# Optimization experiments

Measured on AMD Instinct MI355X. Metric: run time of the kernel, lower is better.

Reference implementation:

```python
import jax, jax.numpy as jnp
import numpy as np

HEADS = 8
HEAD_DIM = 64
IN_DIM = HEADS * HEAD_DIM  # 512
SCALE = HEAD_DIM ** (-0.5)


def _split_heads(t):
    # [b, n, h*d] -> [b, h, n, d]
    b, n, _ = t.shape
    return t.reshape(b, n, HEADS, HEAD_DIM).transpose(0, 2, 1, 3)


def _merge_heads(t):
    # [b, h, n, d] -> [b, n, h*d]
    b, h, n, d = t.shape
    return t.transpose(0, 2, 1, 3).reshape(b, n, h * d)


def setup_inputs() -> dict:
    key = jax.random.key(0)
    ks = jax.random.split(key, 6)
    b, n = 8, 1024
    nv = jax.random.normal(ks[0], (b, n, IN_DIM), dtype=jnp.float32)
    rv = jax.random.normal(ks[1], (b, n, IN_DIM), dtype=jnp.float32)
    s = IN_DIM ** (-0.5)
    W_noise = jax.random.normal(ks[2], (IN_DIM, 2 * IN_DIM), dtype=jnp.float32) * s
    b_noise = jnp.zeros((2 * IN_DIM,), dtype=jnp.float32)
    W_rgb = jax.random.normal(ks[3], (IN_DIM, 2 * IN_DIM), dtype=jnp.float32) * s
    b_rgb = jnp.zeros((2 * IN_DIM,), dtype=jnp.float32)
    return {"nv": nv, "rv": rv, "W_noise": W_noise, "b_noise": b_noise,
            "W_rgb": W_rgb, "b_rgb": b_rgb}


def reference(nv, rv, W_noise, b_noise, W_rgb, b_rgb):
    # qk projections, chunk(2, dim=-1)
    nqk = nv @ W_noise + b_noise                      # [b, n, 2*in_dim]
    noise_q, noise_k = jnp.split(nqk, 2, axis=-1)
    rqk = rv @ W_rgb + b_rgb
    rgb_q, rgb_k = jnp.split(rqk, 2, axis=-1)

    noise_q, noise_k = _split_heads(noise_q), _split_heads(noise_k)  # [b,h,n,d]
    rgb_q, rgb_k = _split_heads(rgb_q), _split_heads(rgb_k)

    attn1 = jnp.einsum('bhnd,bhmd->bhnm', noise_q, rgb_k) * SCALE
    attn2 = jnp.einsum('bhnd,bhmd->bhnm', rgb_q, noise_k) * SCALE

    # NOTE: original uses nn.Softmax(dim=1) => softmax over the HEADS axis.
    attn1 = jax.nn.softmax(attn1, axis=1)
    attn2 = jax.nn.softmax(attn2, axis=1)

    rv_h = _split_heads(rv)  # values are the raw inputs, not projections
    nv_h = _split_heads(nv)

    noise = jnp.einsum('bhnm,bhmd->bhnd', attn1, rv_h)
    rgb = jnp.einsum('bhnm,bhmd->bhnd', attn2, nv_h)

    return (_merge_heads(noise), _merge_heads(rgb))
```

## Files before the change

### kernel.cpp

```cpp
#include <hip/hip_runtime.h>
#include <hip/hip_bf16.h>

typedef __attribute__((ext_vector_type(8))) short short8;
typedef __attribute__((ext_vector_type(4))) short short4v;
typedef __attribute__((ext_vector_type(4))) float float4v;

#define MFMA16(a, b, c) __builtin_amdgcn_mfma_f32_16x16x32_bf16(a, b, c, 0, 0, 0)

__device__ __forceinline__ short f2bf(float f) {
    __hip_bfloat16 hb = __float2bfloat16(f);
    return *reinterpret_cast<short*>(&hb);
}

__global__ __launch_bounds__(256) void proj_kernel(
    const float* __restrict__ nv, const float* __restrict__ rv,
    const float* __restrict__ Wn, const float* __restrict__ bn,
    const float* __restrict__ Wr, const float* __restrict__ br,
    __hip_bfloat16* __restrict__ Qn, __hip_bfloat16* __restrict__ Kn,
    __hip_bfloat16* __restrict__ Qr, __hip_bfloat16* __restrict__ Kr)
{
    const int m0 = blockIdx.x * 64;
    const int c0 = blockIdx.y * 128;
    const int g  = blockIdx.z;
    const float* A    = g ? rv : nv;
    const float* W    = g ? Wr : Wn;
    const float* bias = g ? br : bn;
    __hip_bfloat16* Qd = g ? Qr : Qn;
    __hip_bfloat16* Kd = g ? Kr : Kn;

    __shared__ short Bt[128][40];

    const int t    = threadIdx.x;
    const int lane = t & 63;
    const int w    = t >> 6;
    const int l15  = lane & 15;
    const int lg   = lane >> 4;
    const int kgrp = lg * 8;

    float4v acc[8] = {};
    const int mrow = m0 + w * 16 + l15;

    for (int kk = 0; kk < 512; kk += 32) {
        {
            const int ci = t & 127;
            const int kh = (t >> 7) * 16;
            #pragma unroll
            for (int ki = 0; ki < 16; ++ki) {
                float v = W[(kk + kh + ki) * 1024 + c0 + ci];
                Bt[ci][kh + ki] = f2bf(v);
            }
        }
        __syncthreads();
        short8 afrag;
        {
            const float* ap = A + (size_t)mrow * 512 + kk + kgrp;
            float4 a0 = *reinterpret_cast<const float4*>(ap);
            float4 a1 = *reinterpret_cast<const float4*>(ap + 4);
            short* af = (short*)&afrag;
            af[0] = f2bf(a0.x); af[1] = f2bf(a0.y); af[2] = f2bf(a0.z); af[3] = f2bf(a0.w);
            af[4] = f2bf(a1.x); af[5] = f2bf(a1.y); af[6] = f2bf(a1.z); af[7] = f2bf(a1.w);
        }
        #pragma unroll
        for (int cs = 0; cs < 8; ++cs) {
            short8 bfrag = *reinterpret_cast<const short8*>(&Bt[cs * 16 + l15][kgrp]);
            acc[cs] = MFMA16(afrag, bfrag, acc[cs]);
        }
        __syncthreads();
    }

    #pragma unroll
    for (int cs = 0; cs < 8; ++cs) {
        const int c  = c0 + cs * 16 + l15;
        const bool isK = (c >= 512);
        const int hh = (c >> 6) & 7;
        const int d  = c & 63;
        __hip_bfloat16* dst = isK ? Kd : Qd;
        const float bv = bias[c];
        #pragma unroll
        for (int r = 0; r < 4; ++r) {
            const int m = m0 + w * 16 + lg * 4 + r;
            const int b = m >> 10, n = m & 1023;
            dst[(((size_t)(b * 8 + hh) * 1024 + n) * 64) + d] =
                __float2bfloat16(acc[cs][r] + bv);
        }
    }
}

__global__ __launch_bounds__(256) void transpose_kernel(
    const float* __restrict__ nv, const float* __restrict__ rv,
    __hip_bfloat16* __restrict__ Vtn, __hip_bfloat16* __restrict__ Vtr)
{
    const int ntile = blockIdx.x & 15;
    const int src   = blockIdx.x >> 4;
    const int h     = blockIdx.y;
    const int b     = blockIdx.z;
    const float* V  = src ? rv : nv;
    __hip_bfloat16* Vt = src ? Vtr : Vtn;

    __shared__ short lds[64][72];
    const int t  = threadIdx.x;
    const int n0 = ntile * 64;
    {
        const int i  = t >> 2;
        const int j0 = (t & 3) * 16;
        const float* p = V + ((size_t)(b * 1024) + n0 + i) * 512 + h * 64 + j0;
        #pragma unroll
        for (int jj = 0; jj < 16; ++jj)
            lds[j0 + jj][i] = f2bf(p[jj]);
    }
    __syncthreads();
    {
        const int j  = t >> 2;
        const int i0 = (t & 3) * 16;
        __hip_bfloat16* q = Vt + (((size_t)(b * 8 + h) * 64) + j) * 1024 + n0 + i0;
        short8 v0 = *reinterpret_cast<const short8*>(&lds[j][i0]);
        short8 v1 = *reinterpret_cast<const short8*>(&lds[j][i0 + 8]);
        *reinterpret_cast<short8*>(q)     = v0;
        *reinterpret_cast<short8*>(q + 8) = v1;
    }
}

__global__ __launch_bounds__(512, 2) void attn_kernel(
    const __hip_bfloat16* __restrict__ Qn, const __hip_bfloat16* __restrict__ Kn,
    const __hip_bfloat16* __restrict__ Qr, const __hip_bfloat16* __restrict__ Kr,
    const __hip_bfloat16* __restrict__ Vtn, const __hip_bfloat16* __restrict__ Vtr,
    float* __restrict__ out)
{
    const int combo = blockIdx.x;
    const int bb    = combo & 7;
    const int dir   = combo >> 3;
    const int nt    = blockIdx.y;
    const __hip_bfloat16* Q  = dir ? Qr  : Qn;
    const __hip_bfloat16* K  = dir ? Kn  : Kr;
    const __hip_bfloat16* Vt = dir ? Vtn : Vtr;
    float* O = out + (size_t)dir * (8u * 1024u * 512u);

    const int t    = threadIdx.x;
    const int lane = t & 63;
    const int w    = t >> 6;
    const int iw   = w & 1;
    const int hg   = w >> 1;
    const int h0   = hg * 2;
    const int l15  = lane & 15;
    const int lg   = lane >> 4;

    __shared__ short K_s[2][8 * 32 * 64];
    __shared__ short P_s[8][32][40];
    __shared__ float X_s[2][4][2][512];

    const int n0 = nt * 64;
    const float C = 0.125f * 1.44269504f;

    const __hip_bfloat16* Vb[2] = {
        Vt + (size_t)((bb * 8 + h0)     * 64) * 1024,
        Vt + (size_t)((bb * 8 + h0 + 1) * 64) * 1024 };

    auto stage = [&](int bufn, int mt) {
        #pragma unroll
        for (int i = 0; i < 4; ++i) {
            const int u    = (w * 4 + i) * 64 + lane;
            const int h    = u >> 8;
            const int mr   = (u >> 3) & 31;
            const int slot = (u & 7) ^ (mr & 7);
            const __hip_bfloat16* g =
                K + ((size_t)((bb * 8 + h) * 1024) + mt + mr) * 64 + slot * 8;
            __builtin_amdgcn_global_load_lds(
                (const __attribute__((address_space(1))) unsigned int*)g,
                (__attribute__((address_space(3))) unsigned int*)&K_s[bufn][u * 8],
                16, 0, 0);
        }
    };

    short8 qf[2][2][2];
    #pragma unroll
    for (int ns = 0; ns < 2; ++ns)
        #pragma unroll
        for (int hh = 0; hh < 2; ++hh)
            #pragma unroll
            for (int kc = 0; kc < 2; ++kc)
                qf[ns][hh][kc] = *reinterpret_cast<const short8*>(
                    Q + ((size_t)((bb * 8 + h0 + hh) * 1024) + n0 + ns * 32 + iw * 16 + l15) * 64
                      + kc * 32 + lg * 8);

    float4v oacc[2][2][4] = {};

    stage(0, 0);
    __syncthreads();

    for (int it = 0; it < 32; ++it) {
        const int m0  = it << 5;
        const int buf = it & 1;
        short8 vf[2][4];
        #pragma unroll
        for (int hh = 0; hh < 2; ++hh)
            #pragma unroll
            for (int dd = 0; dd < 4; ++dd)
                vf[hh][dd] = *reinterpret_cast<const short8*>(
                    Vb[hh] + (size_t)(dd * 16 + l15) * 1024 + m0 + lg * 8);
        short8 kf[2][2][2];
        const short* ks = K_s[buf];
        #pragma unroll
        for (int hh = 0; hh < 2; ++hh)
            #pragma unroll
            for (int j = 0; j < 2; ++j) {
                const int mr = j * 16 + l15;
                #pragma unroll
                for (int kc = 0; kc < 2; ++kc)
                    kf[hh][j][kc] = *reinterpret_cast<const short8*>(
                        ks + (h0 + hh) * 2048 + mr * 64
                           + (((kc * 4 + lg) ^ (mr & 7)) * 8));
            }

        #pragma unroll
        for (int ns = 0; ns < 2; ++ns) {
            float4v sacc[2][2] = {};
            #pragma unroll
            for (int hh = 0; hh < 2; ++hh)
                #pragma unroll
                for (int j = 0; j < 2; ++j)
                    #pragma unroll
                    for (int kc = 0; kc < 2; ++kc)
                        sacc[hh][j] = MFMA16(kf[hh][j][kc], qf[ns][hh][kc], sacc[hh][j]);
            float e[2][8];
            float ps[8] = {0.f, 0.f, 0.f, 0.f, 0.f, 0.f, 0.f, 0.f};
            #pragma unroll
            for (int hh = 0; hh < 2; ++hh)
                #pragma unroll
                for (int j = 0; j < 2; ++j)
                    #pragma unroll
                    for (int r = 0; r < 4; ++r) {
                        float ev = exp2f(sacc[hh][j][r] * C);
                        e[hh][j * 4 + r] = ev;
                        ps[j * 4 + r] += ev;
                    }
            #pragma unroll
            for (int p = 0; p < 8; ++p)
                X_s[ns][hg][iw][p * 64 + lane] = ps[p];
            __syncthreads();
            if (ns == 0)
                stage(buf ^ 1, (it < 31) ? m0 + 32 : 0);
            float inv[8];
            #pragma unroll
            for (int p = 0; p < 8; ++p) {
                float tot = ps[p];
                #pragma unroll
                for (int g = 1; g < 4; ++g)
                    tot += X_s[ns][(hg + g) & 3][iw][p * 64 + lane];
                inv[p] = __builtin_amdgcn_rcpf(tot);
            }
            #pragma unroll
            for (int hh = 0; hh < 2; ++hh)
                #pragma unroll
                for (int j = 0; j < 2; ++j) {
                    short4v pk;
                    #pragma unroll
                    for (int r = 0; r < 4; ++r)
                        pk[r] = f2bf(e[hh][j * 4 + r] * inv[j * 4 + r]);
                    *reinterpret_cast<short4v*>(
                        &P_s[h0 + hh][iw * 16 + l15][j * 16 + lg * 4]) = pk;
                }
            #pragma unroll
            for (int hh = 0; hh < 2; ++hh) {
                short8 pf = *reinterpret_cast<const short8*>(
                    &P_s[h0 + hh][iw * 16 + l15][lg * 8]);
                #pragma unroll
                for (int dd = 0; dd < 4; ++dd)
                    oacc[ns][hh][dd] = MFMA16(pf, vf[hh][dd], oacc[ns][hh][dd]);
            }
        }
        __syncthreads();
    }

    #pragma unroll
    for (int ns = 0; ns < 2; ++ns)
        #pragma unroll
        for (int hh = 0; hh < 2; ++hh)
            #pragma unroll
            for (int dd = 0; dd < 4; ++dd)
                #pragma unroll
                for (int r = 0; r < 4; ++r) {
                    const int n = n0 + ns * 32 + iw * 16 + lg * 4 + r;
                    const int d = dd * 16 + l15;
                    O[((size_t)(bb * 1024) + n) * 512 + (h0 + hh) * 64 + d] =
                        oacc[ns][hh][dd][r];
                }
}

extern "C" void kernel_launch(void* const* d_in, const int* in_sizes, int n_in,
                              void* d_out, int out_size, void* d_ws, size_t ws_size,
                              hipStream_t stream) {
    const float* nv = (const float*)d_in[0];
    const float* rv = (const float*)d_in[1];
    const float* Wn = (const float*)d_in[2];
    const float* bn = (const float*)d_in[3];
    const float* Wr = (const float*)d_in[4];
    const float* br = (const float*)d_in[5];
    float* out = (float*)d_out;

    __hip_bfloat16* w = (__hip_bfloat16*)d_ws;
    const size_t E = 8ull * 8 * 1024 * 64;
    __hip_bfloat16* Qn  = w;
    __hip_bfloat16* Kn  = w + E;
    __hip_bfloat16* Qr  = w + 2 * E;
    __hip_bfloat16* Kr  = w + 3 * E;
    __hip_bfloat16* Vtn = w + 4 * E;
    __hip_bfloat16* Vtr = w + 5 * E;

    proj_kernel<<<dim3(128, 8, 2), 256, 0, stream>>>(nv, rv, Wn, bn, Wr, br, Qn, Kn, Qr, Kr);
    transpose_kernel<<<dim3(32, 8, 8), 256, 0, stream>>>(nv, rv, Vtn, Vtr);
    attn_kernel<<<dim3(16, 16), 512, 0, stream>>>(Qn, Kn, Qr, Kr, Vtn, Vtr, out);
}
```

Measured before the change: 173.9 us.

## Pre-convert weights and inputs to bf16, double-buffer projection GEMM, trim attention syncs

Measured after the change: 179.3 us. +3.1%, slower.

```diff
diff --git a/kernel.cpp b/kernel.cpp
--- a/kernel.cpp
+++ b/kernel.cpp
@@ -12,83 +12,42 @@
     return *reinterpret_cast<short*>(&hb);
 }
 
-__global__ __launch_bounds__(256) void proj_kernel(
+__global__ __launch_bounds__(256) void wt_kernel(
+    const float* __restrict__ Wn, const float* __restrict__ Wr,
+    __hip_bfloat16* __restrict__ Wtn, __hip_bfloat16* __restrict__ Wtr)
+{
+    const int c0 = blockIdx.x * 64;
+    const int k0 = blockIdx.y * 64;
+    const int g  = blockIdx.z;
+    const float* W = g ? Wr : Wn;
+    __hip_bfloat16* Wt = g ? Wtr : Wtn;
+
+    __shared__ short lds[64][72];
+    const int t = threadIdx.x;
+    {
+        const int i  = t >> 2;
+        const int j0 = (t & 3) * 16;
+        const float* p = W + (size_t)(k0 + i) * 1024 + c0 + j0;
+        #pragma unroll
+        for (int jj = 0; jj < 16; ++jj)
+            lds[j0 + jj][i] = f2bf(p[jj]);
+    }
+    __syncthreads();
+    {
+        const int j  = t >> 2;
+        const int i0 = (t & 3) * 16;
+        __hip_bfloat16* q = Wt + (size_t)(c0 + j) * 512 + k0 + i0;
+        short8 v0 = *reinterpret_cast<const short8*>(&lds[j][i0]);
+        short8 v1 = *reinterpret_cast<const short8*>(&lds[j][i0 + 8]);
+        *reinterpret_cast<short8*>(q)     = v0;
+        *reinterpret_cast<short8*>(q + 8) = v1;
+    }
+}
+
+__global__ __launch_bounds__(256) void prep_kernel(
     const float* __restrict__ nv, const float* __restrict__ rv,
-    const float* __restrict__ Wn, const float* __restrict__ bn,
-    const float* __restrict__ Wr, const float* __restrict__ br,
-    __hip_bfloat16* __restrict__ Qn, __hip_bfloat16* __restrict__ Kn,
-    __hip_bfloat16* __restrict__ Qr, __hip_bfloat16* __restrict__ Kr)
-{
-    const int m0 = blockIdx.x * 64;
-    const int c0 = blockIdx.y * 128;
-    const int g  = blockIdx.z;
-    const float* A    = g ? rv : nv;
-    const float* W    = g ? Wr : Wn;
-    const float* bias = g ? br : bn;
-    __hip_bfloat16* Qd = g ? Qr : Qn;
-    __hip_bfloat16* Kd = g ? Kr : Kn;
-
-    __shared__ short Bt[128][40];
-
-    const int t    = threadIdx.x;
-    const int lane = t & 63;
-    const int w    = t >> 6;
-    const int l15  = lane & 15;
-    const int lg   = lane >> 4;
-    const int kgrp = lg * 8;
-
-    float4v acc[8] = {};
-    const int mrow = m0 + w * 16 + l15;
-
-    for (int kk = 0; kk < 512; kk += 32) {
-        {
-            const int ci = t & 127;
-            const int kh = (t >> 7) * 16;
-            #pragma unroll
-            for (int ki = 0; ki < 16; ++ki) {
-                float v = W[(kk + kh + ki) * 1024 + c0 + ci];
-                Bt[ci][kh + ki] = f2bf(v);
-            }
-        }
-        __syncthreads();
-        short8 afrag;
-        {
-            const float* ap = A + (size_t)mrow * 512 + kk + kgrp;
-            float4 a0 = *reinterpret_cast<const float4*>(ap);
-            float4 a1 = *reinterpret_cast<const float4*>(ap + 4);
-            short* af = (short*)&afrag;
-            af[0] = f2bf(a0.x); af[1] = f2bf(a0.y); af[2] = f2bf(a0.z); af[3] = f2bf(a0.w);
-            af[4] = f2bf(a1.x); af[5] = f2bf(a1.y); af[6] = f2bf(a1.z); af[7] = f2bf(a1.w);
-        }
-        #pragma unroll
-        for (int cs = 0; cs < 8; ++cs) {
-            short8 bfrag = *reinterpret_cast<const short8*>(&Bt[cs * 16 + l15][kgrp]);
-            acc[cs] = MFMA16(afrag, bfrag, acc[cs]);
-        }
-        __syncthreads();
-    }
-
-    #pragma unroll
-    for (int cs = 0; cs < 8; ++cs) {
-        const int c  = c0 + cs * 16 + l15;
-        const bool isK = (c >= 512);
-        const int hh = (c >> 6) & 7;
-        const int d  = c & 63;
-        __hip_bfloat16* dst = isK ? Kd : Qd;
-        const float bv = bias[c];
-        #pragma unroll
-        for (int r = 0; r < 4; ++r) {
-            const int m = m0 + w * 16 + lg * 4 + r;
-            const int b = m >> 10, n = m & 1023;
-            dst[(((size_t)(b * 8 + hh) * 1024 + n) * 64) + d] =
-                __float2bfloat16(acc[cs][r] + bv);
-        }
-    }
-}
-
-__global__ __launch_bounds__(256) void transpose_kernel(
-    const float* __restrict__ nv, const float* __restrict__ rv,
-    __hip_bfloat16* __restrict__ Vtn, __hip_bfloat16* __restrict__ Vtr)
+    __hip_bfloat16* __restrict__ Vtn, __hip_bfloat16* __restrict__ Vtr,
+    __hip_bfloat16* __restrict__ An,  __hip_bfloat16* __restrict__ Ar)
 {
     const int ntile = blockIdx.x & 15;
     const int src   = blockIdx.x >> 4;
@@ -96,6 +55,7 @@
     const int b     = blockIdx.z;
     const float* V  = src ? rv : nv;
     __hip_bfloat16* Vt = src ? Vtr : Vtn;
+    __hip_bfloat16* Ab = src ? Ar  : An;
 
     __shared__ short lds[64][72];
     const int t  = threadIdx.x;
@@ -104,9 +64,20 @@
         const int i  = t >> 2;
         const int j0 = (t & 3) * 16;
         const float* p = V + ((size_t)(b * 1024) + n0 + i) * 512 + h * 64 + j0;
-        #pragma unroll
-        for (int jj = 0; jj < 16; ++jj)
-            lds[j0 + jj][i] = f2bf(p[jj]);
+        short8 a0, a1;
+        #pragma unroll
+        for (int jj = 0; jj < 8; ++jj) {
+            short x = f2bf(p[jj]);
+            a0[jj] = x; lds[j0 + jj][i] = x;
+        }
+        #pragma unroll
+        for (int jj = 0; jj < 8; ++jj) {
+            short x = f2bf(p[8 + jj]);
+            a1[jj] = x; lds[j0 + 8 + jj][i] = x;
+        }
+        __hip_bfloat16* adst = Ab + ((size_t)(b * 1024) + n0 + i) * 512 + h * 64 + j0;
+        *reinterpret_cast<short8*>(adst)     = a0;
+        *reinterpret_cast<short8*>(adst + 8) = a1;
     }
     __syncthreads();
     {
@@ -117,6 +88,82 @@
         short8 v1 = *reinterpret_cast<const short8*>(&lds[j][i0 + 8]);
         *reinterpret_cast<short8*>(q)     = v0;
         *reinterpret_cast<short8*>(q + 8) = v1;
+    }
+}
+
+__global__ __launch_bounds__(256, 4) void proj_kernel(
+    const __hip_bfloat16* __restrict__ An, const __hip_bfloat16* __restrict__ Ar,
+    const __hip_bfloat16* __restrict__ Wtn, const __hip_bfloat16* __restrict__ Wtr,
+    const float* __restrict__ bn, const float* __restrict__ br,
+    __hip_bfloat16* __restrict__ Qn, __hip_bfloat16* __restrict__ Kn,
+    __hip_bfloat16* __restrict__ Qr, __hip_bfloat16* __restrict__ Kr)
+{
+    const int m0 = blockIdx.x * 64;
+    const int c0 = blockIdx.y * 128;
+    const int g  = blockIdx.z;
+    const __hip_bfloat16* A  = g ? Ar  : An;
+    const __hip_bfloat16* Wt = g ? Wtr : Wtn;
+    const float* bias = g ? br : bn;
+    __hip_bfloat16* Qd = g ? Qr : Qn;
+    __hip_bfloat16* Kd = g ? Kr : Kn;
+
+    __shared__ short Bt[2][4][128][8];
+
+    const int t    = threadIdx.x;
+    const int lane = t & 63;
+    const int w    = t >> 6;
+    const int l15  = lane & 15;
+    const int lg   = lane >> 4;
+
+    auto stage = [&](int buf, int kk) {
+        #pragma unroll
+        for (int rep = 0; rep < 2; ++rep) {
+            const int u = rep * 256 + t;
+            const int s = u >> 7;
+            const int c = u & 127;
+            const __hip_bfloat16* src = Wt + (size_t)(c0 + c) * 512 + kk + s * 8;
+            __builtin_amdgcn_global_load_lds(
+                (const __attribute__((address_space(1))) unsigned int*)src,
+                (__attribute__((address_space(3))) unsigned int*)&Bt[buf][s][c][0],
+                16, 0, 0);
+        }
+    };
+
+    float4v acc[8] = {};
+    const int mrow = m0 + w * 16 + l15;
+
+    stage(0, 0);
+    __syncthreads();
+
+    for (int kk = 0; kk < 512; kk += 32) {
+        const int buf = (kk >> 5) & 1;
+        if (kk < 480) stage(buf ^ 1, kk + 32);
+        short8 afrag = *reinterpret_cast<const short8*>(
+            A + (size_t)mrow * 512 + kk + lg * 8);
+        #pragma unroll
+        for (int cs = 0; cs < 8; ++cs) {
+            short8 bfrag = *reinterpret_cast<const short8*>(
+                &Bt[buf][lg][cs * 16 + l15][0]);
+            acc[cs] = MFMA16(afrag, bfrag, acc[cs]);
+        }
+        __syncthreads();
+    }
+
+    #pragma unroll
+    for (int cs = 0; cs < 8; ++cs) {
+        const int c  = c0 + cs * 16 + l15;
+        const bool isK = (c >= 512);
+        const int hh = (c >> 6) & 7;
+        const int d  = c & 63;
+        __hip_bfloat16* dst = isK ? Kd : Qd;
+        const float bv = bias[c];
+        #pragma unroll
+        for (int r = 0; r < 4; ++r) {
+            const int m = m0 + w * 16 + lg * 4 + r;
+            const int b = m >> 10, n = m & 1023;
+            dst[(((size_t)(b * 8 + hh) * 1024 + n) * 64) + d] =
+                __float2bfloat16(acc[cs][r] + bv);
+        }
     }
 }
 
@@ -146,7 +193,7 @@
 
     __shared__ short K_s[2][8 * 32 * 64];
     __shared__ short P_s[8][32][40];
-    __shared__ float X_s[2][4][2][512];
+    __shared__ float X_s[2][2][4][2][512];
 
     const int n0 = nt * 64;
     const float C = 0.125f * 1.44269504f;
@@ -190,6 +237,8 @@
     for (int it = 0; it < 32; ++it) {
         const int m0  = it << 5;
         const int buf = it & 1;
+        const int par = it & 1;
+        stage(buf ^ 1, (it < 31) ? m0 + 32 : 0);
         short8 vf[2][4];
         #pragma unroll
         for (int hh = 0; hh < 2; ++hh)
@@ -210,7 +259,8 @@
                         ks + (h0 + hh) * 2048 + mr * 64
                            + (((kc * 4 + lg) ^ (mr & 7)) * 8));
             }
-
+        float e[2][2][8];
+        float ps[2][8];
         #pragma unroll
         for (int ns = 0; ns < 2; ++ns) {
             float4v sacc[2][2] = {};
@@ -221,8 +271,8 @@
                     #pragma unroll
                     for (int kc = 0; kc < 2; ++kc)
                         sacc[hh][j] = MFMA16(kf[hh][j][kc], qf[ns][hh][kc], sacc[hh][j]);
-            float e[2][8];
-            float ps[8] = {0.f, 0.f, 0.f, 0.f, 0.f, 0.f, 0.f, 0.f};
+            #pragma unroll
+            for (int p = 0; p < 8; ++p) ps[ns][p] = 0.f;
             #pragma unroll
             for (int hh = 0; hh < 2; ++hh)
                 #pragma unroll
@@ -230,22 +280,23 @@
                     #pragma unroll
                     for (int r = 0; r < 4; ++r) {
                         float ev = exp2f(sacc[hh][j][r] * C);
-                        e[hh][j * 4 + r] = ev;
-                        ps[j * 4 + r] += ev;
+                        e[ns][hh][j * 4 + r] = ev;
+                        ps[ns][j * 4 + r] += ev;
                     }
             #pragma unroll
             for (int p = 0; p < 8; ++p)
-                X_s[ns][hg][iw][p * 64 + lane] = ps[p];
-            __syncthreads();
-            if (ns == 0)
-                stage(buf ^ 1, (it < 31) ? m0 + 32 : 0);
+                X_s[par][ns][hg][iw][p * 64 + lane] = ps[ns][p];
+        }
+        __syncthreads();
+        #pragma unroll
+        for (int ns = 0; ns < 2; ++ns) {
             float inv[8];
             #pragma unroll
             for (int p = 0; p < 8; ++p) {
-                float tot = ps[p];
+                float tot = ps[ns][p];
                 #pragma unroll
                 for (int g = 1; g < 4; ++g)
-                    tot += X_s[ns][(hg + g) & 3][iw][p * 64 + lane];
+                    tot += X_s[par][ns][(hg + g) & 3][iw][p * 64 + lane];
                 inv[p] = __builtin_amdgcn_rcpf(tot);
             }
             #pragma unroll
@@ -255,7 +306,7 @@
                     short4v pk;
                     #pragma unroll
                     for (int r = 0; r < 4; ++r)
-                        pk[r] = f2bf(e[hh][j * 4 + r] * inv[j * 4 + r]);
+                        pk[r] = f2bf(e[ns][hh][j * 4 + r] * inv[j * 4 + r]);
                     *reinterpret_cast<short4v*>(
                         &P_s[h0 + hh][iw * 16 + l15][j * 16 + lg * 4]) = pk;
                 }
@@ -268,7 +319,6 @@
                     oacc[ns][hh][dd] = MFMA16(pf, vf[hh][dd], oacc[ns][hh][dd]);
             }
         }
-        __syncthreads();
     }
 
     #pragma unroll
@@ -305,8 +355,14 @@
     __hip_bfloat16* Kr  = w + 3 * E;
     __hip_bfloat16* Vtn = w + 4 * E;
     __hip_bfloat16* Vtr = w + 5 * E;
-
-    proj_kernel<<<dim3(128, 8, 2), 256, 0, stream>>>(nv, rv, Wn, bn, Wr, br, Qn, Kn, Qr, Kr);
-    transpose_kernel<<<dim3(32, 8, 8), 256, 0, stream>>>(nv, rv, Vtn, Vtr);
+    __hip_bfloat16* An  = w + 6 * E;
+    __hip_bfloat16* Ar  = w + 7 * E;
+    __hip_bfloat16* Wtn = w + 8 * E;
+    __hip_bfloat16* Wtr = w + 8 * E + 512 * 1024;
+
+    wt_kernel  <<<dim3(16, 8, 2), 256, 0, stream>>>(Wn, Wr, Wtn, Wtr);
+    prep_kernel<<<dim3(32, 8, 8), 256, 0, stream>>>(nv, rv, Vtn, Vtr, An, Ar);
+    proj_kernel<<<dim3(128, 8, 2), 256, 0, stream>>>(An, Ar, Wtn, Wtr, bn, br,
+                                                     Qn, Kn, Qr, Kr);
     attn_kernel<<<dim3(16, 16), 512, 0, stream>>>(Qn, Kn, Qr, Kr, Vtn, Vtr, out);
 }
```
